# Optimization experiments

Hardware: AMD Instinct MI355X
Metric: run time of the kernel (lower is better)

## Reference

```python
import jax, jax.numpy as jnp
import numpy as np

N = 4096   # num ROIs across the batch (sgdet: ~8 images x 512 proposals)
H = 256    # rl_input_size == rl_hidden_size (hard-coded in __init__)
C = 151    # Visual Genome object classes incl. background


def setup_inputs() -> dict:
    key = jax.random.key(0)
    ks = jax.random.split(key, 7)
    prepro_feat = jax.random.normal(ks[0], (N, H), jnp.float32)
    d = jax.random.uniform(ks[1], (N, C), jnp.float32)
    obj_distributions = d / d.sum(-1, keepdims=True)  # softmax-like class probs
    co_occour = jax.random.uniform(ks[2], (C, C), jnp.float32)
    W_sub = jax.random.normal(ks[3], (H, H), jnp.float32) / np.sqrt(H)
    b_sub = jnp.zeros((H,), jnp.float32)
    W_obj = jax.random.normal(ks[4], (H, H), jnp.float32) / np.sqrt(H)
    b_obj = jnp.zeros((H,), jnp.float32)
    w_scores = jax.random.normal(ks[5], (3 * H + 3,), jnp.float32) / np.sqrt(3 * H + 3)
    b_scores = jnp.zeros((), jnp.float32)
    return dict(prepro_feat=prepro_feat, obj_distributions=obj_distributions,
                co_occour=co_occour, W_sub=W_sub, b_sub=b_sub,
                W_obj=W_obj, b_obj=b_obj, w_scores=w_scores, b_scores=b_scores)


def reference(prepro_feat, obj_distributions, co_occour, W_sub, b_sub,
              W_obj, b_obj, w_scores, b_scores):
    n = prepro_feat.shape[0]
    h = W_sub.shape[1]
    # label_scores = co_occour.sum(1)
    label_scores = co_occour.sum(1)                                   # [C]
    # rl_sub/rl_obj Linear + ReLU. In the torch expand, pair (i,j) uses sub[j], obj[i].
    sub = jax.nn.relu(prepro_feat @ W_sub + b_sub)                    # [N,H]
    obj = jax.nn.relu(prepro_feat @ W_obj + b_obj)                    # [N,H]
    # pair_score[i,j] = sum_{a,b} dist[j,a] * dist[i,b] * co[a,b]  (detached)
    pair_score = jax.lax.stop_gradient(
        jnp.einsum('ja,ab,ib->ij', obj_distributions, co_occour, obj_distributions))  # [N,N]
    s = jax.lax.stop_gradient(obj_distributions @ label_scores)       # [N]
    sub_score = s[None, :]   # varies along j
    obj_score = s[:, None]   # varies along i
    # rl_scores Linear over concat(sub*obj, sub, obj, pair, sub_score, obj_score),
    # decomposed exactly into its blocks (avoids the [N,N,3H+3] intermediate).
    w_mul, w_s, w_o = w_scores[:h], w_scores[h:2 * h], w_scores[2 * h:3 * h]
    w_ps, w_ss, w_os = w_scores[3 * h], w_scores[3 * h + 1], w_scores[3 * h + 2]
    pair_out = ((obj * w_mul) @ sub.T                                 # [i,j] = sum_h obj[i,h]*sub[j,h]*w_mul[h]
                + (sub @ w_s)[None, :]
                + (obj @ w_o)[:, None]
                + w_ps * pair_score + w_ss * sub_score + w_os * obj_score
                + b_scores)                                           # [N,N]
    pair_gates = jax.nn.sigmoid(pair_out).reshape(-1, 1)              # [N*N, 1]
    return pair_gates
```

## Files before the change

kernel.cpp:

```cpp
#include <hip/hip_runtime.h>
#include <hip/hip_bf16.h>
#include <math.h>

#define N_DIM 4096
#define H_DIM 256
#define C_DIM 151
#define KP    448
#define KT    160

typedef unsigned short ushort_t;
typedef __attribute__((ext_vector_type(8))) short bf16x8;
typedef __attribute__((ext_vector_type(4))) float f32x4;

#define WSB_PPACK  0
#define WSB_WT     2097152
#define WSB_DPACK  2359296
#define WSB_COT    3670016
#define WSB_PART   3731456
#define WSB_SPART  3993600
#define WSB_APACK  4091904
#define WSB_BPACK  7761920

#define GLL(src, dst) __builtin_amdgcn_global_load_lds( \
    (const __attribute__((address_space(1))) void*)(src), \
    (__attribute__((address_space(3))) void*)(dst), 16, 0, 0)

__global__ __launch_bounds__(256) void k_cvt(
    const float* __restrict__ P, const float* __restrict__ Ws,
    const float* __restrict__ Wo, const float* __restrict__ D,
    const float* __restrict__ co, const float* __restrict__ wsc,
    __hip_bfloat16* __restrict__ Pp, __hip_bfloat16* __restrict__ Wt,
    __hip_bfloat16* __restrict__ Dpack, __hip_bfloat16* __restrict__ coT,
    __hip_bfloat16* __restrict__ Apack) {
    __shared__ float shbuf[64 * C_DIM];
    const int t = threadIdx.x;
    const int bid = blockIdx.x;
    if (bid < 512) {
        int idx = (bid * 256 + t) * 8;
        float4 a = *(const float4*)(P + idx);
        float4 b = *(const float4*)(P + idx + 4);
        __hip_bfloat16 h[8];
        h[0] = __float2bfloat16(a.x); h[1] = __float2bfloat16(a.y);
        h[2] = __float2bfloat16(a.z); h[3] = __float2bfloat16(a.w);
        h[4] = __float2bfloat16(b.x); h[5] = __float2bfloat16(b.y);
        h[6] = __float2bfloat16(b.z); h[7] = __float2bfloat16(b.w);
        *(bf16x8*)&Pp[idx] = *(bf16x8*)h;
    } else if (bid < 544) {
        const int b  = bid - 512;
        const int k0 = (b & 3) * 64;
        const int h0 = ((b >> 2) & 3) * 64;
        const int z  = b >> 4;
        const float* W = z ? Wo : Ws;
        #pragma unroll
        for (int q = 0; q < 4; ++q) {
            int r = (t >> 4) + q * 16;
            int c = (t & 15) * 4;
            float4 f = *(const float4*)&W[(size_t)(k0 + r) * H_DIM + h0 + c];
            shbuf[r * 65 + c] = f.x; shbuf[r * 65 + c + 1] = f.y;
            shbuf[r * 65 + c + 2] = f.z; shbuf[r * 65 + c + 3] = f.w;
        }
        __syncthreads();
        #pragma unroll
        for (int q = 0; q < 2; ++q) {
            int idx = t + q * 256;
            int h   = idx >> 3;
            int kc  = idx & 7;
            __hip_bfloat16 u[8];
            #pragma unroll
            for (int j = 0; j < 8; ++j)
                u[j] = __float2bfloat16(shbuf[(kc * 8 + j) * 65 + h]);
            *(bf16x8*)&Wt[((size_t)z * H_DIM + h0 + h) * H_DIM + k0 + kc * 8] = *(bf16x8*)u;
        }
    } else if (bid < 608) {
        const int b  = bid - 544;
        const int i0 = b * 64;
        for (int idx = t; idx < 64 * C_DIM; idx += 256)
            shbuf[idx] = D[(size_t)i0 * C_DIM + idx];
        __syncthreads();
        const float wps = wsc[768];
        for (int o = t; o < 64 * (KT / 8); o += 256) {
            int r = o / (KT / 8), ch = o % (KT / 8);
            __hip_bfloat16 u[8];
            #pragma unroll
            for (int j = 0; j < 8; ++j) {
                int k = ch * 8 + j;
                u[j] = __float2bfloat16(k < C_DIM ? shbuf[r * C_DIM + k] : 0.f);
            }
            *(bf16x8*)&Dpack[(size_t)(i0 + r) * KT + ch * 8] = *(bf16x8*)u;
        }
        for (int o = t; o < 64 * 24; o += 256) {
            int r = o / 24, ch = o % 24;
            __hip_bfloat16 u[8];
            #pragma unroll
            for (int j = 0; j < 8; ++j) {
                int c = ch * 8 + j;
                u[j] = __float2bfloat16(c < C_DIM ? wps * shbuf[r * C_DIM + c] : 0.f);
            }
            *(bf16x8*)&Apack[(size_t)(i0 + r) * KP + H_DIM + ch * 8] = *(bf16x8*)u;
        }
    } else {
        const int q  = bid - 608;
        const int a0 = (q % 3) * 64;
        const int c0 = (q / 3) * 64;
        for (int o = t; o < 64 * 64; o += 256) {
            int r = o >> 6, c = o & 63;
            float v = 0.f;
            if (a0 + r < C_DIM && c0 + c < C_DIM)
                v = co[(size_t)(a0 + r) * C_DIM + c0 + c];
            shbuf[r * 65 + c] = v;
        }
        __syncthreads();
        const int nch = (a0 == 128) ? 4 : 8;
        for (int o = t; o < 64 * 8; o += 256) {
            int cl = o >> 3, ch = o & 7;
            if (ch < nch) {
                __hip_bfloat16 u[8];
                #pragma unroll
                for (int j = 0; j < 8; ++j)
                    u[j] = __float2bfloat16(shbuf[(ch * 8 + j) * 65 + cl]);
                *(bf16x8*)&coT[(size_t)(c0 + cl) * KT + a0 + ch * 8] = *(bf16x8*)u;
            }
        }
    }
}

__global__ __launch_bounds__(256) void k_tailmm(
    const ushort_t* __restrict__ Dpack, const ushort_t* __restrict__ coT,
    __hip_bfloat16* __restrict__ Bpack, float* __restrict__ spart) {
    const int t = threadIdx.x;
    const int w = t >> 6, l = t & 63;
    const int wr = w >> 1, wc = w & 1;
    const int lr = l & 15, g = l >> 4;
    const int j0 = blockIdx.x * 64;
    const int i0 = blockIdx.y * 64;

    bf16x8 a[2][5], b[2][5];
    #pragma unroll
    for (int m = 0; m < 2; ++m) {
        const ushort_t* ap = Dpack + (size_t)(i0 + wr * 32 + m * 16 + lr) * KT + g * 8;
        #pragma unroll
        for (int ks = 0; ks < 5; ++ks) a[m][ks] = *(const bf16x8*)(ap + ks * 32);
    }
    #pragma unroll
    for (int n = 0; n < 2; ++n) {
        const ushort_t* bp = coT + (size_t)(j0 + wc * 32 + n * 16 + lr) * KT + g * 8;
        #pragma unroll
        for (int ks = 0; ks < 5; ++ks) b[n][ks] = *(const bf16x8*)(bp + ks * 32);
    }

    f32x4 acc[2][2];
    #pragma unroll
    for (int m = 0; m < 2; ++m)
        #pragma unroll
        for (int n = 0; n < 2; ++n) acc[m][n] = f32x4{0.f, 0.f, 0.f, 0.f};
    #pragma unroll
    for (int ks = 0; ks < 5; ++ks)
        #pragma unroll
        for (int m = 0; m < 2; ++m)
            #pragma unroll
            for (int n = 0; n < 2; ++n)
                acc[m][n] = __builtin_amdgcn_mfma_f32_16x16x32_bf16(
                    a[m][ks], b[n][ks], acc[m][n], 0, 0, 0);

    float* sp = spart + (size_t)(blockIdx.x * 2 + wc) * N_DIM;
    #pragma unroll
    for (int m = 0; m < 2; ++m) {
        float p[4] = {0.f, 0.f, 0.f, 0.f};
        #pragma unroll
        for (int n = 0; n < 2; ++n) {
            int col = j0 + wc * 32 + n * 16 + lr;
            #pragma unroll
            for (int r = 0; r < 4; ++r) {
                int i = i0 + wr * 32 + m * 16 + g * 4 + r;
                float v = acc[m][n][r];
                Bpack[(size_t)i * KP + H_DIM + col] = __float2bfloat16(v);
                p[r] += v;
            }
        }
        #pragma unroll
        for (int r = 0; r < 4; ++r) {
            p[r] += __shfl_xor(p[r], 1);
            p[r] += __shfl_xor(p[r], 2);
            p[r] += __shfl_xor(p[r], 4);
            p[r] += __shfl_xor(p[r], 8);
        }
        if (lr == 0)
            #pragma unroll
            for (int r = 0; r < 4; ++r)
                sp[i0 + wr * 32 + m * 16 + g * 4 + r] = p[r];
    }
}

__global__ __launch_bounds__(256) void k_subobj(
    const ushort_t* __restrict__ Pp, const ushort_t* __restrict__ Wt,
    const float* __restrict__ bsub, const float* __restrict__ bobj,
    const float* __restrict__ wsc,
    __hip_bfloat16* __restrict__ Apack, __hip_bfloat16* __restrict__ Bpack,
    float* __restrict__ part) {
    const int hblk = blockIdx.x;
    const int i0   = blockIdx.y * 128;
    const int z    = blockIdx.z;
    const int j0   = hblk * 64;
    const float* bias = z ? bobj : bsub;
    const ushort_t* Wz = Wt + (size_t)z * H_DIM * H_DIM;

    __shared__ ushort_t As[128 * 256];
    __shared__ ushort_t Bs[64 * 256];

    const int t = threadIdx.x;
    const int w = t >> 6, l = t & 63;
    const int wr = w >> 1, wc = w & 1;
    const int lr = l & 15, g = l >> 4;

    #pragma unroll
    for (int r_ = 0; r_ < 16; ++r_) {
        int idx = t + r_ * 256, row = idx >> 5, cl = idx & 31;
        int cs = cl ^ (row & 7);
        GLL(Pp + (size_t)(i0 + row) * H_DIM + cs * 8, &As[idx * 8]);
    }
    #pragma unroll
    for (int r_ = 0; r_ < 8; ++r_) {
        int idx = t + r_ * 256, row = idx >> 5, cl = idx & 31;
        int cs = cl ^ (row & 7);
        GLL(Wz + (size_t)(j0 + row) * H_DIM + cs * 8, &Bs[idx * 8]);
    }
    __syncthreads();

    f32x4 acc[4][2];
    #pragma unroll
    for (int m = 0; m < 4; ++m)
        #pragma unroll
        for (int n = 0; n < 2; ++n) acc[m][n] = f32x4{0.f, 0.f, 0.f, 0.f};

    #pragma unroll
    for (int ks2 = 0; ks2 < 8; ++ks2) {
        bf16x8 a[4], b[2];
        int c = ks2 * 4 + g;
        #pragma unroll
        for (int m = 0; m < 4; ++m) {
            int Rl = wr * 64 + m * 16 + lr;
            int cl = c ^ (Rl & 7);
            a[m] = *(const bf16x8*)&As[(Rl * 32 + cl) * 8];
        }
        #pragma unroll
        for (int n = 0; n < 2; ++n) {
            int Rl = wc * 32 + n * 16 + lr;
            int cl = c ^ (Rl & 7);
            b[n] = *(const bf16x8*)&Bs[(Rl * 32 + cl) * 8];
        }
        #pragma unroll
        for (int m = 0; m < 4; ++m)
            #pragma unroll
            for (int n = 0; n < 2; ++n)
                acc[m][n] = __builtin_amdgcn_mfma_f32_16x16x32_bf16(
                    a[m], b[n], acc[m][n], 0, 0, 0);
    }

    int hn[2]; float bb[2], wse[2], wmu[2];
    #pragma unroll
    for (int n = 0; n < 2; ++n) {
        hn[n]  = j0 + wc * 32 + n * 16 + lr;
        bb[n]  = bias[hn[n]];
        wse[n] = wsc[(z ? 512 : 256) + hn[n]];
        wmu[n] = wsc[hn[n]];
    }
    float* partq = part + (size_t)(z * 8 + hblk * 2 + wc) * N_DIM;
    #pragma unroll
    for (int m = 0; m < 4; ++m) {
        float p[4] = {0.f, 0.f, 0.f, 0.f};
        #pragma unroll
        for (int n = 0; n < 2; ++n)
            #pragma unroll
            for (int r = 0; r < 4; ++r) {
                float v = acc[m][n][r] + bb[n];
                v = v > 0.f ? v : 0.f;
                int i = i0 + wr * 64 + m * 16 + g * 4 + r;
                if (z) Apack[(size_t)i * KP + hn[n]] = __float2bfloat16(v * wmu[n]);
                else   Bpack[(size_t)i * KP + hn[n]] = __float2bfloat16(v);
                p[r] += v * wse[n];
            }
        #pragma unroll
        for (int r = 0; r < 4; ++r) {
            p[r] += __shfl_xor(p[r], 1);
            p[r] += __shfl_xor(p[r], 2);
            p[r] += __shfl_xor(p[r], 4);
            p[r] += __shfl_xor(p[r], 8);
        }
        if (lr == 0)
            #pragma unroll
            for (int r = 0; r < 4; ++r)
                partq[i0 + wr * 64 + m * 16 + g * 4 + r] = p[r];
    }
}

__global__ __launch_bounds__(512, 2) void k_main(
    const ushort_t* __restrict__ Apack, const ushort_t* __restrict__ Bpack,
    const float* __restrict__ part, const float* __restrict__ spart,
    const float* __restrict__ wsc, const float* __restrict__ bsc,
    float* __restrict__ out) {
    __shared__ ushort_t pool[2][2][256 * 64];
    __shared__ float rbS[256], cbS[256];

    const int t = threadIdx.x;
    const int w = t >> 6, l = t & 63;
    const int wm = w >> 2, wn = w & 3;
    const int lr = l & 15, g = l >> 4;
    const int bid = blockIdx.x;
    const int swz = (bid & 7) * 32 + (bid >> 3);
    const int i0 = (swz >> 4) * 256;
    const int j0 = (swz & 15) * 256;

#define K_STAGE(buf, ks) do {                                                   \
    _Pragma("unroll")                                                           \
    for (int r_ = 0; r_ < 4; ++r_) {                                            \
        int idx_ = t + r_ * 512, row_ = idx_ >> 3, cl_ = idx_ & 7;              \
        int cs_ = cl_ ^ (row_ & 7);                                             \
        GLL(Apack + (size_t)(i0+row_)*KP + (ks)*64 + cs_*8, &pool[buf][0][idx_*8]); \
        GLL(Bpack + (size_t)(j0+row_)*KP + (ks)*64 + cs_*8, &pool[buf][1][idx_*8]); \
    }                                                                           \
} while (0)

    K_STAGE(0, 0);
    if (t < 256) {
        int i = i0 + t; float r = 0.f, si = 0.f;
        #pragma unroll
        for (int q = 8; q < 16; ++q) r += part[(size_t)q * N_DIM + i];
        #pragma unroll
        for (int q = 0; q < 6; ++q) si += spart[(size_t)q * N_DIM + i];
        rbS[t] = r + wsc[770] * si;
    } else {
        int j = j0 + (t - 256); float c = 0.f, sj = 0.f;
        #pragma unroll
        for (int q = 0; q < 8; ++q) c += part[(size_t)q * N_DIM + j];
        #pragma unroll
        for (int q = 0; q < 6; ++q) sj += spart[(size_t)q * N_DIM + j];
        cbS[t - 256] = c + wsc[769] * sj + bsc[0];
    }
    __syncthreads();

    f32x4 acc[8][4];
    #pragma unroll
    for (int m = 0; m < 8; ++m)
        #pragma unroll
        for (int n = 0; n < 4; ++n) acc[m][n] = f32x4{0.f, 0.f, 0.f, 0.f};

    for (int ks = 0; ks < 7; ++ks) {
        const int cur = ks & 1;
        if (ks < 6) K_STAGE(cur ^ 1, ks + 1);
        #pragma unroll
        for (int ks2 = 0; ks2 < 2; ++ks2) {
            bf16x8 a[8], b[4];
            int c = ks2 * 4 + g;
            #pragma unroll
            for (int m = 0; m < 8; ++m) {
                int Rl = wm * 128 + m * 16 + lr;
                int cl = c ^ (Rl & 7);
                a[m] = *(const bf16x8*)&pool[cur][0][(Rl * 8 + cl) * 8];
            }
            #pragma unroll
            for (int n = 0; n < 4; ++n) {
                int Rl = wn * 64 + n * 16 + lr;
                int cl = c ^ (Rl & 7);
                b[n] = *(const bf16x8*)&pool[cur][1][(Rl * 8 + cl) * 8];
            }
            #pragma unroll
            for (int m = 0; m < 8; ++m)
                #pragma unroll
                for (int n = 0; n < 4; ++n)
                    acc[m][n] = __builtin_amdgcn_mfma_f32_16x16x32_bf16(
                        a[m], b[n], acc[m][n], 0, 0, 0);
        }
        __syncthreads();
    }
#undef K_STAGE

    float cbv[4];
    #pragma unroll
    for (int n = 0; n < 4; ++n) cbv[n] = cbS[wn * 64 + n * 16 + lr];
    float* OutS = (float*)pool;
    #pragma unroll
    for (int m = 0; m < 8; ++m) {
        #pragma unroll
        for (int n = 0; n < 4; ++n) {
            #pragma unroll
            for (int r = 0; r < 4; ++r) {
                float rb = rbS[wm * 128 + m * 16 + g * 4 + r];
                float v  = acc[m][n][r] + rb + cbv[n];
                float e  = __expf(-v);
                OutS[(wm * 16 + g * 4 + r) * 260 + wn * 64 + n * 16 + lr] =
                    __builtin_amdgcn_rcpf(1.0f + e);
            }
        }
        __syncthreads();
        {
            int rl = t >> 4, c16 = t & 15;
            int gr = i0 + (rl >> 4) * 128 + m * 16 + (rl & 15);
            float* op = out + (size_t)gr * N_DIM + j0;
            const float* rp = OutS + rl * 260;
            #pragma unroll
            for (int k = 0; k < 4; ++k) {
                float4 v4 = *(const float4*)(rp + (c16 + 16 * k) * 4);
                *(float4*)(op + (c16 + 16 * k) * 4) = v4;
            }
        }
        __syncthreads();
    }
}

extern "C" void kernel_launch(void* const* d_in, const int* in_sizes, int n_in,
                              void* d_out, int out_size, void* d_ws, size_t ws_size,
                              hipStream_t stream) {
    const float* prepro = (const float*)d_in[0];
    const float* D      = (const float*)d_in[1];
    const float* co     = (const float*)d_in[2];
    const float* Wsub   = (const float*)d_in[3];
    const float* bsub   = (const float*)d_in[4];
    const float* Wobj   = (const float*)d_in[5];
    const float* bobj   = (const float*)d_in[6];
    const float* wsc    = (const float*)d_in[7];
    const float* bsc    = (const float*)d_in[8];
    float* out = (float*)d_out;

    char* ws = (char*)d_ws;
    __hip_bfloat16* Ppack = (__hip_bfloat16*)(ws + WSB_PPACK);
    __hip_bfloat16* Wt    = (__hip_bfloat16*)(ws + WSB_WT);
    __hip_bfloat16* Dpack = (__hip_bfloat16*)(ws + WSB_DPACK);
    __hip_bfloat16* coT   = (__hip_bfloat16*)(ws + WSB_COT);
    float* part  = (float*)(ws + WSB_PART);
    float* spart = (float*)(ws + WSB_SPART);
    __hip_bfloat16* Apack = (__hip_bfloat16*)(ws + WSB_APACK);
    __hip_bfloat16* Bpack = (__hip_bfloat16*)(ws + WSB_BPACK);

    k_cvt<<<617, 256, 0, stream>>>(prepro, Wsub, Wobj, D, co, wsc,
                                   Ppack, Wt, Dpack, coT, Apack);
    k_tailmm<<<dim3(3, 64), 256, 0, stream>>>(
        (const ushort_t*)Dpack, (const ushort_t*)coT, Bpack, spart);
    k_subobj<<<dim3(4, N_DIM / 128, 2), 256, 0, stream>>>(
        (const ushort_t*)Ppack, (const ushort_t*)Wt, bsub, bobj, wsc,
        Apack, Bpack, part);
    k_main<<<256, 512, 0, stream>>>(
        (const ushort_t*)Apack, (const ushort_t*)Bpack, part, spart, wsc, bsc, out);
}
```

Measured before the change: 49.53 us.

## Merge tail and sub/obj GEMM kernels, shrink main tile to 256x128

Fuses the pair-score tail GEMM and the sub/obj linear kernels into one launch, using block-index ranges to pick the role. This removes a kernel launch and lets the two independent GEMMs run side by side. The main kernel tile changes from 256x256 to 256x128 with 512 blocks, which halves accumulator registers and LDS per block so more blocks fit per CU, at the cost of more redundant A-tile loads. The rewrite also drops the minimum-blocks hint in launch_bounds.

```diff
diff --git a/kernel.cpp b/kernel.cpp
--- a/kernel.cpp
+++ b/kernel.cpp
@@ -124,199 +124,202 @@
     }
 }
 
-__global__ __launch_bounds__(256) void k_tailmm(
+__global__ __launch_bounds__(256) void k_mid(
+    const ushort_t* __restrict__ Pp, const ushort_t* __restrict__ Wt,
     const ushort_t* __restrict__ Dpack, const ushort_t* __restrict__ coT,
-    __hip_bfloat16* __restrict__ Bpack, float* __restrict__ spart) {
+    const float* __restrict__ bsub, const float* __restrict__ bobj,
+    const float* __restrict__ wsc,
+    __hip_bfloat16* __restrict__ Apack, __hip_bfloat16* __restrict__ Bpack,
+    float* __restrict__ part, float* __restrict__ spart) {
+    __shared__ ushort_t As[128 * 256];
+    __shared__ ushort_t Bs[64 * 256];
+
     const int t = threadIdx.x;
     const int w = t >> 6, l = t & 63;
     const int wr = w >> 1, wc = w & 1;
     const int lr = l & 15, g = l >> 4;
-    const int j0 = blockIdx.x * 64;
-    const int i0 = blockIdx.y * 64;
-
-    bf16x8 a[2][5], b[2][5];
-    #pragma unroll
-    for (int m = 0; m < 2; ++m) {
-        const ushort_t* ap = Dpack + (size_t)(i0 + wr * 32 + m * 16 + lr) * KT + g * 8;
-        #pragma unroll
-        for (int ks = 0; ks < 5; ++ks) a[m][ks] = *(const bf16x8*)(ap + ks * 32);
-    }
-    #pragma unroll
-    for (int n = 0; n < 2; ++n) {
-        const ushort_t* bp = coT + (size_t)(j0 + wc * 32 + n * 16 + lr) * KT + g * 8;
-        #pragma unroll
-        for (int ks = 0; ks < 5; ++ks) b[n][ks] = *(const bf16x8*)(bp + ks * 32);
-    }
-
-    f32x4 acc[2][2];
-    #pragma unroll
-    for (int m = 0; m < 2; ++m)
-        #pragma unroll
-        for (int n = 0; n < 2; ++n) acc[m][n] = f32x4{0.f, 0.f, 0.f, 0.f};
-    #pragma unroll
-    for (int ks = 0; ks < 5; ++ks)
+    const int bid = blockIdx.x;
+
+    if (bid < 256) {
+        const int hblk = bid & 3;
+        const int i0   = ((bid >> 2) & 31) * 128;
+        const int z    = bid >> 7;
+        const int j0   = hblk * 64;
+        const float* bias = z ? bobj : bsub;
+        const ushort_t* Wz = Wt + (size_t)z * H_DIM * H_DIM;
+
+        #pragma unroll
+        for (int r_ = 0; r_ < 16; ++r_) {
+            int idx = t + r_ * 256, row = idx >> 5, cl = idx & 31;
+            int cs = cl ^ (row & 7);
+            GLL(Pp + (size_t)(i0 + row) * H_DIM + cs * 8, &As[idx * 8]);
+        }
+        #pragma unroll
+        for (int r_ = 0; r_ < 8; ++r_) {
+            int idx = t + r_ * 256, row = idx >> 5, cl = idx & 31;
+            int cs = cl ^ (row & 7);
+            GLL(Wz + (size_t)(j0 + row) * H_DIM + cs * 8, &Bs[idx * 8]);
+        }
+        __syncthreads();
+
+        f32x4 acc[4][2];
+        #pragma unroll
+        for (int m = 0; m < 4; ++m)
+            #pragma unroll
+            for (int n = 0; n < 2; ++n) acc[m][n] = f32x4{0.f, 0.f, 0.f, 0.f};
+
+        #pragma unroll
+        for (int ks2 = 0; ks2 < 8; ++ks2) {
+            bf16x8 a[4], b[2];
+            int c = ks2 * 4 + g;
+            #pragma unroll
+            for (int m = 0; m < 4; ++m) {
+                int Rl = wr * 64 + m * 16 + lr;
+                int cl = c ^ (Rl & 7);
+                a[m] = *(const bf16x8*)&As[(Rl * 32 + cl) * 8];
+            }
+            #pragma unroll
+            for (int n = 0; n < 2; ++n) {
+                int Rl = wc * 32 + n * 16 + lr;
+                int cl = c ^ (Rl & 7);
+                b[n] = *(const bf16x8*)&Bs[(Rl * 32 + cl) * 8];
+            }
+            #pragma unroll
+            for (int m = 0; m < 4; ++m)
+                #pragma unroll
+                for (int n = 0; n < 2; ++n)
+                    acc[m][n] = __builtin_amdgcn_mfma_f32_16x16x32_bf16(
+                        a[m], b[n], acc[m][n], 0, 0, 0);
+        }
+
+        int hn[2]; float bb[2], wse[2], wmu[2];
+        #pragma unroll
+        for (int n = 0; n < 2; ++n) {
+            hn[n]  = j0 + wc * 32 + n * 16 + lr;
+            bb[n]  = bias[hn[n]];
+            wse[n] = wsc[(z ? 512 : 256) + hn[n]];
+            wmu[n] = wsc[hn[n]];
+        }
+        float* partq = part + (size_t)(z * 8 + hblk * 2 + wc) * N_DIM;
+        #pragma unroll
+        for (int m = 0; m < 4; ++m) {
+            float p[4] = {0.f, 0.f, 0.f, 0.f};
+            #pragma unroll
+            for (int n = 0; n < 2; ++n)
+                #pragma unroll
+                for (int r = 0; r < 4; ++r) {
+                    float v = acc[m][n][r] + bb[n];
+                    v = v > 0.f ? v : 0.f;
+                    int i = i0 + wr * 64 + m * 16 + g * 4 + r;
+                    if (z) Apack[(size_t)i * KP + hn[n]] = __float2bfloat16(v * wmu[n]);
+                    else   Bpack[(size_t)i * KP + hn[n]] = __float2bfloat16(v);
+                    p[r] += v * wse[n];
+                }
+            #pragma unroll
+            for (int r = 0; r < 4; ++r) {
+                p[r] += __shfl_xor(p[r], 1);
+                p[r] += __shfl_xor(p[r], 2);
+                p[r] += __shfl_xor(p[r], 4);
+                p[r] += __shfl_xor(p[r], 8);
+            }
+            if (lr == 0)
+                #pragma unroll
+                for (int r = 0; r < 4; ++r)
+                    partq[i0 + wr * 64 + m * 16 + g * 4 + r] = p[r];
+        }
+    } else {
+        const int q  = bid - 256;
+        const int j0 = (q % 3) * 64;
+        const int i0 = (q / 3) * 64;
+
+        bf16x8 a[2][5], b[2][5];
+        #pragma unroll
+        for (int m = 0; m < 2; ++m) {
+            const ushort_t* ap = Dpack + (size_t)(i0 + wr * 32 + m * 16 + lr) * KT + g * 8;
+            #pragma unroll
+            for (int ks = 0; ks < 5; ++ks) a[m][ks] = *(const bf16x8*)(ap + ks * 32);
+        }
+        #pragma unroll
+        for (int n = 0; n < 2; ++n) {
+            const ushort_t* bp = coT + (size_t)(j0 + wc * 32 + n * 16 + lr) * KT + g * 8;
+            #pragma unroll
+            for (int ks = 0; ks < 5; ++ks) b[n][ks] = *(const bf16x8*)(bp + ks * 32);
+        }
+
+        f32x4 acc[2][2];
         #pragma unroll
         for (int m = 0; m < 2; ++m)
             #pragma unroll
-            for (int n = 0; n < 2; ++n)
-                acc[m][n] = __builtin_amdgcn_mfma_f32_16x16x32_bf16(
-                    a[m][ks], b[n][ks], acc[m][n], 0, 0, 0);
-
-    float* sp = spart + (size_t)(blockIdx.x * 2 + wc) * N_DIM;
-    #pragma unroll
-    for (int m = 0; m < 2; ++m) {
-        float p[4] = {0.f, 0.f, 0.f, 0.f};
-        #pragma unroll
-        for (int n = 0; n < 2; ++n) {
-            int col = j0 + wc * 32 + n * 16 + lr;
+            for (int n = 0; n < 2; ++n) acc[m][n] = f32x4{0.f, 0.f, 0.f, 0.f};
+        #pragma unroll
+        for (int ks = 0; ks < 5; ++ks)
+            #pragma unroll
+            for (int m = 0; m < 2; ++m)
+                #pragma unroll
+                for (int n = 0; n < 2; ++n)
+                    acc[m][n] = __builtin_amdgcn_mfma_f32_16x16x32_bf16(
+                        a[m][ks], b[n][ks], acc[m][n], 0, 0, 0);
+
+        float* sp = spart + (size_t)((q % 3) * 2 + wc) * N_DIM;
+        #pragma unroll
+        for (int m = 0; m < 2; ++m) {
+            float p[4] = {0.f, 0.f, 0.f, 0.f};
+            #pragma unroll
+            for (int n = 0; n < 2; ++n) {
+                int col = j0 + wc * 32 + n * 16 + lr;
+                #pragma unroll
+                for (int r = 0; r < 4; ++r) {
+                    int i = i0 + wr * 32 + m * 16 + g * 4 + r;
+                    float v = acc[m][n][r];
+                    Bpack[(size_t)i * KP + H_DIM + col] = __float2bfloat16(v);
+                    p[r] += v;
+                }
+            }
             #pragma unroll
             for (int r = 0; r < 4; ++r) {
-                int i = i0 + wr * 32 + m * 16 + g * 4 + r;
-                float v = acc[m][n][r];
-                Bpack[(size_t)i * KP + H_DIM + col] = __float2bfloat16(v);
-                p[r] += v;
-            }
-        }
-        #pragma unroll
-        for (int r = 0; r < 4; ++r) {
-            p[r] += __shfl_xor(p[r], 1);
-            p[r] += __shfl_xor(p[r], 2);
-            p[r] += __shfl_xor(p[r], 4);
-            p[r] += __shfl_xor(p[r], 8);
-        }
-        if (lr == 0)
-            #pragma unroll
-            for (int r = 0; r < 4; ++r)
-                sp[i0 + wr * 32 + m * 16 + g * 4 + r] = p[r];
+                p[r] += __shfl_xor(p[r], 1);
+                p[r] += __shfl_xor(p[r], 2);
+                p[r] += __shfl_xor(p[r], 4);
+                p[r] += __shfl_xor(p[r], 8);
+            }
+            if (lr == 0)
+                #pragma unroll
+                for (int r = 0; r < 4; ++r)
+                    sp[i0 + wr * 32 + m * 16 + g * 4 + r] = p[r];
+        }
     }
 }
 
-__global__ __launch_bounds__(256) void k_subobj(
-    const ushort_t* __restrict__ Pp, const ushort_t* __restrict__ Wt,
-    const float* __restrict__ bsub, const float* __restrict__ bobj,
-    const float* __restrict__ wsc,
-    __hip_bfloat16* __restrict__ Apack, __hip_bfloat16* __restrict__ Bpack,
-    float* __restrict__ part) {
-    const int hblk = blockIdx.x;
-    const int i0   = blockIdx.y * 128;
-    const int z    = blockIdx.z;
-    const int j0   = hblk * 64;
-    const float* bias = z ? bobj : bsub;
-    const ushort_t* Wz = Wt + (size_t)z * H_DIM * H_DIM;
-
-    __shared__ ushort_t As[128 * 256];
-    __shared__ ushort_t Bs[64 * 256];
-
-    const int t = threadIdx.x;
-    const int w = t >> 6, l = t & 63;
-    const int wr = w >> 1, wc = w & 1;
-    const int lr = l & 15, g = l >> 4;
-
-    #pragma unroll
-    for (int r_ = 0; r_ < 16; ++r_) {
-        int idx = t + r_ * 256, row = idx >> 5, cl = idx & 31;
-        int cs = cl ^ (row & 7);
-        GLL(Pp + (size_t)(i0 + row) * H_DIM + cs * 8, &As[idx * 8]);
-    }
-    #pragma unroll
-    for (int r_ = 0; r_ < 8; ++r_) {
-        int idx = t + r_ * 256, row = idx >> 5, cl = idx & 31;
-        int cs = cl ^ (row & 7);
-        GLL(Wz + (size_t)(j0 + row) * H_DIM + cs * 8, &Bs[idx * 8]);
-    }
-    __syncthreads();
-
-    f32x4 acc[4][2];
-    #pragma unroll
-    for (int m = 0; m < 4; ++m)
-        #pragma unroll
-        for (int n = 0; n < 2; ++n) acc[m][n] = f32x4{0.f, 0.f, 0.f, 0.f};
-
-    #pragma unroll
-    for (int ks2 = 0; ks2 < 8; ++ks2) {
-        bf16x8 a[4], b[2];
-        int c = ks2 * 4 + g;
-        #pragma unroll
-        for (int m = 0; m < 4; ++m) {
-            int Rl = wr * 64 + m * 16 + lr;
-            int cl = c ^ (Rl & 7);
-            a[m] = *(const bf16x8*)&As[(Rl * 32 + cl) * 8];
-        }
-        #pragma unroll
-        for (int n = 0; n < 2; ++n) {
-            int Rl = wc * 32 + n * 16 + lr;
-            int cl = c ^ (Rl & 7);
-            b[n] = *(const bf16x8*)&Bs[(Rl * 32 + cl) * 8];
-        }
-        #pragma unroll
-        for (int m = 0; m < 4; ++m)
-            #pragma unroll
-            for (int n = 0; n < 2; ++n)
-                acc[m][n] = __builtin_amdgcn_mfma_f32_16x16x32_bf16(
-                    a[m], b[n], acc[m][n], 0, 0, 0);
-    }
-
-    int hn[2]; float bb[2], wse[2], wmu[2];
-    #pragma unroll
-    for (int n = 0; n < 2; ++n) {
-        hn[n]  = j0 + wc * 32 + n * 16 + lr;
-        bb[n]  = bias[hn[n]];
-        wse[n] = wsc[(z ? 512 : 256) + hn[n]];
-        wmu[n] = wsc[hn[n]];
-    }
-    float* partq = part + (size_t)(z * 8 + hblk * 2 + wc) * N_DIM;
-    #pragma unroll
-    for (int m = 0; m < 4; ++m) {
-        float p[4] = {0.f, 0.f, 0.f, 0.f};
-        #pragma unroll
-        for (int n = 0; n < 2; ++n)
-            #pragma unroll
-            for (int r = 0; r < 4; ++r) {
-                float v = acc[m][n][r] + bb[n];
-                v = v > 0.f ? v : 0.f;
-                int i = i0 + wr * 64 + m * 16 + g * 4 + r;
-                if (z) Apack[(size_t)i * KP + hn[n]] = __float2bfloat16(v * wmu[n]);
-                else   Bpack[(size_t)i * KP + hn[n]] = __float2bfloat16(v);
-                p[r] += v * wse[n];
-            }
-        #pragma unroll
-        for (int r = 0; r < 4; ++r) {
-            p[r] += __shfl_xor(p[r], 1);
-            p[r] += __shfl_xor(p[r], 2);
-            p[r] += __shfl_xor(p[r], 4);
-            p[r] += __shfl_xor(p[r], 8);
-        }
-        if (lr == 0)
-            #pragma unroll
-            for (int r = 0; r < 4; ++r)
-                partq[i0 + wr * 64 + m * 16 + g * 4 + r] = p[r];
-    }
-}
-
-__global__ __launch_bounds__(512, 2) void k_main(
+__global__ __launch_bounds__(512) void k_main(
     const ushort_t* __restrict__ Apack, const ushort_t* __restrict__ Bpack,
     const float* __restrict__ part, const float* __restrict__ spart,
     const float* __restrict__ wsc, const float* __restrict__ bsc,
     float* __restrict__ out) {
-    __shared__ ushort_t pool[2][2][256 * 64];
-    __shared__ float rbS[256], cbS[256];
+    __shared__ ushort_t pa[2][256 * 64];
+    __shared__ ushort_t pb[2][128 * 64];
+    __shared__ float rbS[256], cbS[128];
 
     const int t = threadIdx.x;
     const int w = t >> 6, l = t & 63;
-    const int wm = w >> 2, wn = w & 3;
+    const int wm = w >> 1, wn = w & 1;
     const int lr = l & 15, g = l >> 4;
     const int bid = blockIdx.x;
-    const int swz = (bid & 7) * 32 + (bid >> 3);
-    const int i0 = (swz >> 4) * 256;
-    const int j0 = (swz & 15) * 256;
+    const int wgid = (bid & 7) * 64 + (bid >> 3);
+    const int i0 = (wgid >> 5) * 256;
+    const int j0 = (wgid & 31) * 128;
 
 #define K_STAGE(buf, ks) do {                                                   \
     _Pragma("unroll")                                                           \
     for (int r_ = 0; r_ < 4; ++r_) {                                            \
         int idx_ = t + r_ * 512, row_ = idx_ >> 3, cl_ = idx_ & 7;              \
         int cs_ = cl_ ^ (row_ & 7);                                             \
-        GLL(Apack + (size_t)(i0+row_)*KP + (ks)*64 + cs_*8, &pool[buf][0][idx_*8]); \
-        GLL(Bpack + (size_t)(j0+row_)*KP + (ks)*64 + cs_*8, &pool[buf][1][idx_*8]); \
+        GLL(Apack + (size_t)(i0+row_)*KP + (ks)*64 + cs_*8, &pa[buf][idx_*8]);  \
+    }                                                                           \
+    _Pragma("unroll")                                                           \
+    for (int r_ = 0; r_ < 2; ++r_) {                                            \
+        int idx_ = t + r_ * 512, row_ = idx_ >> 3, cl_ = idx_ & 7;              \
+        int cs_ = cl_ ^ (row_ & 7);                                             \
+        GLL(Bpack + (size_t)(j0+row_)*KP + (ks)*64 + cs_*8, &pb[buf][idx_*8]);  \
     }                                                                           \
 } while (0)
 
@@ -328,7 +331,7 @@
         #pragma unroll
         for (int q = 0; q < 6; ++q) si += spart[(size_t)q * N_DIM + i];
         rbS[t] = r + wsc[770] * si;
-    } else {
+    } else if (t < 384) {
         int j = j0 + (t - 256); float c = 0.f, sj = 0.f;
         #pragma unroll
         for (int q = 0; q < 8; ++q) c += part[(size_t)q * N_DIM + j];
@@ -338,9 +341,9 @@
     }
     __syncthreads();
 
-    f32x4 acc[8][4];
+    f32x4 acc[4][4];
     #pragma unroll
-    for (int m = 0; m < 8; ++m)
+    for (int m = 0; m < 4; ++m)
         #pragma unroll
         for (int n = 0; n < 4; ++n) acc[m][n] = f32x4{0.f, 0.f, 0.f, 0.f};
 
@@ -349,22 +352,22 @@
         if (ks < 6) K_STAGE(cur ^ 1, ks + 1);
         #pragma unroll
         for (int ks2 = 0; ks2 < 2; ++ks2) {
-            bf16x8 a[8], b[4];
+            bf16x8 a[4], b[4];
             int c = ks2 * 4 + g;
             #pragma unroll
-            for (int m = 0; m < 8; ++m) {
-                int Rl = wm * 128 + m * 16 + lr;
+            for (int m = 0; m < 4; ++m) {
+                int Rl = wm * 64 + m * 16 + lr;
                 int cl = c ^ (Rl & 7);
-                a[m] = *(const bf16x8*)&pool[cur][0][(Rl * 8 + cl) * 8];
+                a[m] = *(const bf16x8*)&pa[cur][(Rl * 8 + cl) * 8];
             }
             #pragma unroll
             for (int n = 0; n < 4; ++n) {
                 int Rl = wn * 64 + n * 16 + lr;
                 int cl = c ^ (Rl & 7);
-                b[n] = *(const bf16x8*)&pool[cur][1][(Rl * 8 + cl) * 8];
-            }
-            #pragma unroll
-            for (int m = 0; m < 8; ++m)
+                b[n] = *(const bf16x8*)&pb[cur][(Rl * 8 + cl) * 8];
+            }
+            #pragma unroll
+            for (int m = 0; m < 4; ++m)
                 #pragma unroll
                 for (int n = 0; n < 4; ++n)
                     acc[m][n] = __builtin_amdgcn_mfma_f32_16x16x32_bf16(
@@ -377,30 +380,30 @@
     float cbv[4];
     #pragma unroll
     for (int n = 0; n < 4; ++n) cbv[n] = cbS[wn * 64 + n * 16 + lr];
-    float* OutS = (float*)pool;
+    float* OutS = (float*)pa;
     #pragma unroll
-    for (int m = 0; m < 8; ++m) {
+    for (int m = 0; m < 4; ++m) {
         #pragma unroll
         for (int n = 0; n < 4; ++n) {
             #pragma unroll
             for (int r = 0; r < 4; ++r) {
-                float rb = rbS[wm * 128 + m * 16 + g * 4 + r];
+                float rb = rbS[wm * 64 + m * 16 + g * 4 + r];
                 float v  = acc[m][n][r] + rb + cbv[n];
                 float e  = __expf(-v);
-                OutS[(wm * 16 + g * 4 + r) * 260 + wn * 64 + n * 16 + lr] =
+                OutS[(wm * 16 + g * 4 + r) * 132 + wn * 64 + n * 16 + lr] =
                     __builtin_amdgcn_rcpf(1.0f + e);
             }
         }
         __syncthreads();
         {
-            int rl = t >> 4, c16 = t & 15;
-            int gr = i0 + (rl >> 4) * 128 + m * 16 + (rl & 15);
+            int rl = t >> 3, c8 = t & 7;
+            int gr = i0 + (rl >> 4) * 64 + m * 16 + (rl & 15);
             float* op = out + (size_t)gr * N_DIM + j0;
-            const float* rp = OutS + rl * 260;
+            const float* rp = OutS + rl * 132;
             #pragma unroll
             for (int k = 0; k < 4; ++k) {
-                float4 v4 = *(const float4*)(rp + (c16 + 16 * k) * 4);
-                *(float4*)(op + (c16 + 16 * k) * 4) = v4;
+                float4 v4 = *(const float4*)(rp + (c8 + 8 * k) * 4);
+                *(float4*)(op + (c8 + 8 * k) * 4) = v4;
             }
         }
         __syncthreads();
@@ -433,11 +436,10 @@
 
     k_cvt<<<617, 256, 0, stream>>>(prepro, Wsub, Wobj, D, co, wsc,
                                    Ppack, Wt, Dpack, coT, Apack);
-    k_tailmm<<<dim3(3, 64), 256, 0, stream>>>(
-        (const ushort_t*)Dpack, (const ushort_t*)coT, Bpack, spart);
-    k_subobj<<<dim3(4, N_DIM / 128, 2), 256, 0, stream>>>(
-        (const ushort_t*)Ppack, (const ushort_t*)Wt, bsub, bobj, wsc,
-        Apack, Bpack, part);
-    k_main<<<256, 512, 0, stream>>>(
+    k_mid<<<448, 256, 0, stream>>>(
+        (const ushort_t*)Ppack, (const ushort_t*)Wt,
+        (const ushort_t*)Dpack, (const ushort_t*)coT,
+        bsub, bobj, wsc, Apack, Bpack, part, spart);
+    k_main<<<512, 512, 0, stream>>>(
         (const ushort_t*)Apack, (const ushort_t*)Bpack, part, spart, wsc, bsc, out);
 }
```

Result: slower. 54.15 us (+9.3%).

## Merge tail and sub/obj GEMM kernels; use explicit waitcnt barriers in main loop

Applied to the files above, without the earlier changes.

Merges the pair-score tail GEMM and the sub/obj linear GEMM into one kernel, split by block index, so a single launch covers both and their blocks can run concurrently. In the main kernel it replaces __syncthreads with explicit vmcnt waits plus raw s_barrier and sched_barrier, and peels the last K step out of the loop. The goal is to drop a launch gap and let the next tile's loads stay in flight during compute. The hand-counted vmcnt(8) ties correctness to the exact number of loads each K_STAGE issues, so any change in that count would break the synchronisation.

```diff
diff --git a/kernel.cpp b/kernel.cpp
--- a/kernel.cpp
+++ b/kernel.cpp
@@ -124,172 +124,169 @@
     }
 }
 
-__global__ __launch_bounds__(256) void k_tailmm(
+__global__ __launch_bounds__(256) void k_mid(
+    const ushort_t* __restrict__ Pp, const ushort_t* __restrict__ Wt,
     const ushort_t* __restrict__ Dpack, const ushort_t* __restrict__ coT,
-    __hip_bfloat16* __restrict__ Bpack, float* __restrict__ spart) {
+    const float* __restrict__ bsub, const float* __restrict__ bobj,
+    const float* __restrict__ wsc,
+    __hip_bfloat16* __restrict__ Apack, __hip_bfloat16* __restrict__ Bpack,
+    float* __restrict__ part, float* __restrict__ spart) {
+    __shared__ ushort_t As[128 * 256];
+    __shared__ ushort_t Bs[64 * 256];
+
     const int t = threadIdx.x;
     const int w = t >> 6, l = t & 63;
     const int wr = w >> 1, wc = w & 1;
     const int lr = l & 15, g = l >> 4;
-    const int j0 = blockIdx.x * 64;
-    const int i0 = blockIdx.y * 64;
-
-    bf16x8 a[2][5], b[2][5];
-    #pragma unroll
-    for (int m = 0; m < 2; ++m) {
-        const ushort_t* ap = Dpack + (size_t)(i0 + wr * 32 + m * 16 + lr) * KT + g * 8;
-        #pragma unroll
-        for (int ks = 0; ks < 5; ++ks) a[m][ks] = *(const bf16x8*)(ap + ks * 32);
-    }
-    #pragma unroll
-    for (int n = 0; n < 2; ++n) {
-        const ushort_t* bp = coT + (size_t)(j0 + wc * 32 + n * 16 + lr) * KT + g * 8;
-        #pragma unroll
-        for (int ks = 0; ks < 5; ++ks) b[n][ks] = *(const bf16x8*)(bp + ks * 32);
-    }
-
-    f32x4 acc[2][2];
-    #pragma unroll
-    for (int m = 0; m < 2; ++m)
-        #pragma unroll
-        for (int n = 0; n < 2; ++n) acc[m][n] = f32x4{0.f, 0.f, 0.f, 0.f};
-    #pragma unroll
-    for (int ks = 0; ks < 5; ++ks)
+    const int bid = blockIdx.x;
+
+    if (bid < 256) {
+        const int hblk = bid & 3;
+        const int i0   = ((bid >> 2) & 31) * 128;
+        const int z    = bid >> 7;
+        const int j0   = hblk * 64;
+        const float* bias = z ? bobj : bsub;
+        const ushort_t* Wz = Wt + (size_t)z * H_DIM * H_DIM;
+
+        #pragma unroll
+        for (int r_ = 0; r_ < 16; ++r_) {
+            int idx = t + r_ * 256, row = idx >> 5, cl = idx & 31;
+            int cs = cl ^ (row & 7);
+            GLL(Pp + (size_t)(i0 + row) * H_DIM + cs * 8, &As[idx * 8]);
+        }
+        #pragma unroll
+        for (int r_ = 0; r_ < 8; ++r_) {
+            int idx = t + r_ * 256, row = idx >> 5, cl = idx & 31;
+            int cs = cl ^ (row & 7);
+            GLL(Wz + (size_t)(j0 + row) * H_DIM + cs * 8, &Bs[idx * 8]);
+        }
+        __syncthreads();
+
+        f32x4 acc[4][2];
+        #pragma unroll
+        for (int m = 0; m < 4; ++m)
+            #pragma unroll
+            for (int n = 0; n < 2; ++n) acc[m][n] = f32x4{0.f, 0.f, 0.f, 0.f};
+
+        #pragma unroll
+        for (int ks2 = 0; ks2 < 8; ++ks2) {
+            bf16x8 a[4], b[2];
+            int c = ks2 * 4 + g;
+            #pragma unroll
+            for (int m = 0; m < 4; ++m) {
+                int Rl = wr * 64 + m * 16 + lr;
+                int cl = c ^ (Rl & 7);
+                a[m] = *(const bf16x8*)&As[(Rl * 32 + cl) * 8];
+            }
+            #pragma unroll
+            for (int n = 0; n < 2; ++n) {
+                int Rl = wc * 32 + n * 16 + lr;
+                int cl = c ^ (Rl & 7);
+                b[n] = *(const bf16x8*)&Bs[(Rl * 32 + cl) * 8];
+            }
+            #pragma unroll
+            for (int m = 0; m < 4; ++m)
+                #pragma unroll
+                for (int n = 0; n < 2; ++n)
+                    acc[m][n] = __builtin_amdgcn_mfma_f32_16x16x32_bf16(
+                        a[m], b[n], acc[m][n], 0, 0, 0);
+        }
+
+        int hn[2]; float bb[2], wse[2], wmu[2];
+        #pragma unroll
+        for (int n = 0; n < 2; ++n) {
+            hn[n]  = j0 + wc * 32 + n * 16 + lr;
+            bb[n]  = bias[hn[n]];
+            wse[n] = wsc[(z ? 512 : 256) + hn[n]];
+            wmu[n] = wsc[hn[n]];
+        }
+        float* partq = part + (size_t)(z * 8 + hblk * 2 + wc) * N_DIM;
+        #pragma unroll
+        for (int m = 0; m < 4; ++m) {
+            float p[4] = {0.f, 0.f, 0.f, 0.f};
+            #pragma unroll
+            for (int n = 0; n < 2; ++n)
+                #pragma unroll
+                for (int r = 0; r < 4; ++r) {
+                    float v = acc[m][n][r] + bb[n];
+                    v = v > 0.f ? v : 0.f;
+                    int i = i0 + wr * 64 + m * 16 + g * 4 + r;
+                    if (z) Apack[(size_t)i * KP + hn[n]] = __float2bfloat16(v * wmu[n]);
+                    else   Bpack[(size_t)i * KP + hn[n]] = __float2bfloat16(v);
+                    p[r] += v * wse[n];
+                }
+            #pragma unroll
+            for (int r = 0; r < 4; ++r) {
+                p[r] += __shfl_xor(p[r], 1);
+                p[r] += __shfl_xor(p[r], 2);
+                p[r] += __shfl_xor(p[r], 4);
+                p[r] += __shfl_xor(p[r], 8);
+            }
+            if (lr == 0)
+                #pragma unroll
+                for (int r = 0; r < 4; ++r)
+                    partq[i0 + wr * 64 + m * 16 + g * 4 + r] = p[r];
+        }
+    } else {
+        const int q  = bid - 256;
+        const int j0 = (q % 3) * 64;
+        const int i0 = (q / 3) * 64;
+
+        bf16x8 a[2][5], b[2][5];
+        #pragma unroll
+        for (int m = 0; m < 2; ++m) {
+            const ushort_t* ap = Dpack + (size_t)(i0 + wr * 32 + m * 16 + lr) * KT + g * 8;
+            #pragma unroll
+            for (int ks = 0; ks < 5; ++ks) a[m][ks] = *(const bf16x8*)(ap + ks * 32);
+        }
+        #pragma unroll
+        for (int n = 0; n < 2; ++n) {
+            const ushort_t* bp = coT + (size_t)(j0 + wc * 32 + n * 16 + lr) * KT + g * 8;
+            #pragma unroll
+            for (int ks = 0; ks < 5; ++ks) b[n][ks] = *(const bf16x8*)(bp + ks * 32);
+        }
+
+        f32x4 acc[2][2];
         #pragma unroll
         for (int m = 0; m < 2; ++m)
             #pragma unroll
-            for (int n = 0; n < 2; ++n)
-                acc[m][n] = __builtin_amdgcn_mfma_f32_16x16x32_bf16(
-                    a[m][ks], b[n][ks], acc[m][n], 0, 0, 0);
-
-    float* sp = spart + (size_t)(blockIdx.x * 2 + wc) * N_DIM;
-    #pragma unroll
-    for (int m = 0; m < 2; ++m) {
-        float p[4] = {0.f, 0.f, 0.f, 0.f};
-        #pragma unroll
-        for (int n = 0; n < 2; ++n) {
-            int col = j0 + wc * 32 + n * 16 + lr;
+            for (int n = 0; n < 2; ++n) acc[m][n] = f32x4{0.f, 0.f, 0.f, 0.f};
+        #pragma unroll
+        for (int ks = 0; ks < 5; ++ks)
+            #pragma unroll
+            for (int m = 0; m < 2; ++m)
+                #pragma unroll
+                for (int n = 0; n < 2; ++n)
+                    acc[m][n] = __builtin_amdgcn_mfma_f32_16x16x32_bf16(
+                        a[m][ks], b[n][ks], acc[m][n], 0, 0, 0);
+
+        float* sp = spart + (size_t)((q % 3) * 2 + wc) * N_DIM;
+        #pragma unroll
+        for (int m = 0; m < 2; ++m) {
+            float p[4] = {0.f, 0.f, 0.f, 0.f};
+            #pragma unroll
+            for (int n = 0; n < 2; ++n) {
+                int col = j0 + wc * 32 + n * 16 + lr;
+                #pragma unroll
+                for (int r = 0; r < 4; ++r) {
+                    int i = i0 + wr * 32 + m * 16 + g * 4 + r;
+                    float v = acc[m][n][r];
+                    Bpack[(size_t)i * KP + H_DIM + col] = __float2bfloat16(v);
+                    p[r] += v;
+                }
+            }
             #pragma unroll
             for (int r = 0; r < 4; ++r) {
-                int i = i0 + wr * 32 + m * 16 + g * 4 + r;
-                float v = acc[m][n][r];
-                Bpack[(size_t)i * KP + H_DIM + col] = __float2bfloat16(v);
-                p[r] += v;
-            }
-        }
-        #pragma unroll
-        for (int r = 0; r < 4; ++r) {
-            p[r] += __shfl_xor(p[r], 1);
-            p[r] += __shfl_xor(p[r], 2);
-            p[r] += __shfl_xor(p[r], 4);
-            p[r] += __shfl_xor(p[r], 8);
-        }
-        if (lr == 0)
-            #pragma unroll
-            for (int r = 0; r < 4; ++r)
-                sp[i0 + wr * 32 + m * 16 + g * 4 + r] = p[r];
-    }
-}
-
-__global__ __launch_bounds__(256) void k_subobj(
-    const ushort_t* __restrict__ Pp, const ushort_t* __restrict__ Wt,
-    const float* __restrict__ bsub, const float* __restrict__ bobj,
-    const float* __restrict__ wsc,
-    __hip_bfloat16* __restrict__ Apack, __hip_bfloat16* __restrict__ Bpack,
-    float* __restrict__ part) {
-    const int hblk = blockIdx.x;
-    const int i0   = blockIdx.y * 128;
-    const int z    = blockIdx.z;
-    const int j0   = hblk * 64;
-    const float* bias = z ? bobj : bsub;
-    const ushort_t* Wz = Wt + (size_t)z * H_DIM * H_DIM;
-
-    __shared__ ushort_t As[128 * 256];
-    __shared__ ushort_t Bs[64 * 256];
-
-    const int t = threadIdx.x;
-    const int w = t >> 6, l = t & 63;
-    const int wr = w >> 1, wc = w & 1;
-    const int lr = l & 15, g = l >> 4;
-
-    #pragma unroll
-    for (int r_ = 0; r_ < 16; ++r_) {
-        int idx = t + r_ * 256, row = idx >> 5, cl = idx & 31;
-        int cs = cl ^ (row & 7);
-        GLL(Pp + (size_t)(i0 + row) * H_DIM + cs * 8, &As[idx * 8]);
-    }
-    #pragma unroll
-    for (int r_ = 0; r_ < 8; ++r_) {
-        int idx = t + r_ * 256, row = idx >> 5, cl = idx & 31;
-        int cs = cl ^ (row & 7);
-        GLL(Wz + (size_t)(j0 + row) * H_DIM + cs * 8, &Bs[idx * 8]);
-    }
-    __syncthreads();
-
-    f32x4 acc[4][2];
-    #pragma unroll
-    for (int m = 0; m < 4; ++m)
-        #pragma unroll
-        for (int n = 0; n < 2; ++n) acc[m][n] = f32x4{0.f, 0.f, 0.f, 0.f};
-
-    #pragma unroll
-    for (int ks2 = 0; ks2 < 8; ++ks2) {
-        bf16x8 a[4], b[2];
-        int c = ks2 * 4 + g;
-        #pragma unroll
-        for (int m = 0; m < 4; ++m) {
-            int Rl = wr * 64 + m * 16 + lr;
-            int cl = c ^ (Rl & 7);
-            a[m] = *(const bf16x8*)&As[(Rl * 32 + cl) * 8];
-        }
-        #pragma unroll
-        for (int n = 0; n < 2; ++n) {
-            int Rl = wc * 32 + n * 16 + lr;
-            int cl = c ^ (Rl & 7);
-            b[n] = *(const bf16x8*)&Bs[(Rl * 32 + cl) * 8];
-        }
-        #pragma unroll
-        for (int m = 0; m < 4; ++m)
-            #pragma unroll
-            for (int n = 0; n < 2; ++n)
-                acc[m][n] = __builtin_amdgcn_mfma_f32_16x16x32_bf16(
-                    a[m], b[n], acc[m][n], 0, 0, 0);
-    }
-
-    int hn[2]; float bb[2], wse[2], wmu[2];
-    #pragma unroll
-    for (int n = 0; n < 2; ++n) {
-        hn[n]  = j0 + wc * 32 + n * 16 + lr;
-        bb[n]  = bias[hn[n]];
-        wse[n] = wsc[(z ? 512 : 256) + hn[n]];
-        wmu[n] = wsc[hn[n]];
-    }
-    float* partq = part + (size_t)(z * 8 + hblk * 2 + wc) * N_DIM;
-    #pragma unroll
-    for (int m = 0; m < 4; ++m) {
-        float p[4] = {0.f, 0.f, 0.f, 0.f};
-        #pragma unroll
-        for (int n = 0; n < 2; ++n)
-            #pragma unroll
-            for (int r = 0; r < 4; ++r) {
-                float v = acc[m][n][r] + bb[n];
-                v = v > 0.f ? v : 0.f;
-                int i = i0 + wr * 64 + m * 16 + g * 4 + r;
-                if (z) Apack[(size_t)i * KP + hn[n]] = __float2bfloat16(v * wmu[n]);
-                else   Bpack[(size_t)i * KP + hn[n]] = __float2bfloat16(v);
-                p[r] += v * wse[n];
-            }
-        #pragma unroll
-        for (int r = 0; r < 4; ++r) {
-            p[r] += __shfl_xor(p[r], 1);
-            p[r] += __shfl_xor(p[r], 2);
-            p[r] += __shfl_xor(p[r], 4);
-            p[r] += __shfl_xor(p[r], 8);
-        }
-        if (lr == 0)
-            #pragma unroll
-            for (int r = 0; r < 4; ++r)
-                partq[i0 + wr * 64 + m * 16 + g * 4 + r] = p[r];
+                p[r] += __shfl_xor(p[r], 1);
+                p[r] += __shfl_xor(p[r], 2);
+                p[r] += __shfl_xor(p[r], 4);
+                p[r] += __shfl_xor(p[r], 8);
+            }
+            if (lr == 0)
+                #pragma unroll
+                for (int r = 0; r < 4; ++r)
+                    sp[i0 + wr * 32 + m * 16 + g * 4 + r] = p[r];
+        }
     }
 }
 
@@ -320,6 +317,32 @@
     }                                                                           \
 } while (0)
 
+#define K_COMPUTE(cur) do {                                                     \
+    _Pragma("unroll")                                                           \
+    for (int ks2 = 0; ks2 < 2; ++ks2) {                                         \
+        bf16x8 a[8], b[4];                                                      \
+        int c = ks2 * 4 + g;                                                    \
+        _Pragma("unroll")                                                       \
+        for (int m = 0; m < 8; ++m) {                                           \
+            int Rl = wm * 128 + m * 16 + lr;                                    \
+            int cl = c ^ (Rl & 7);                                              \
+            a[m] = *(const bf16x8*)&pool[cur][0][(Rl * 8 + cl) * 8];            \
+        }                                                                       \
+        _Pragma("unroll")                                                       \
+        for (int n = 0; n < 4; ++n) {                                           \
+            int Rl = wn * 64 + n * 16 + lr;                                     \
+            int cl = c ^ (Rl & 7);                                              \
+            b[n] = *(const bf16x8*)&pool[cur][1][(Rl * 8 + cl) * 8];            \
+        }                                                                       \
+        _Pragma("unroll")                                                       \
+        for (int m = 0; m < 8; ++m)                                             \
+            _Pragma("unroll")                                                   \
+            for (int n = 0; n < 4; ++n)                                         \
+                acc[m][n] = __builtin_amdgcn_mfma_f32_16x16x32_bf16(            \
+                    a[m], b[n], acc[m][n], 0, 0, 0);                            \
+    }                                                                           \
+} while (0)
+
     K_STAGE(0, 0);
     if (t < 256) {
         int i = i0 + t; float r = 0.f, si = 0.f;
@@ -344,35 +367,24 @@
         #pragma unroll
         for (int n = 0; n < 4; ++n) acc[m][n] = f32x4{0.f, 0.f, 0.f, 0.f};
 
-    for (int ks = 0; ks < 7; ++ks) {
+    for (int ks = 0; ks < 6; ++ks) {
         const int cur = ks & 1;
-        if (ks < 6) K_STAGE(cur ^ 1, ks + 1);
-        #pragma unroll
-        for (int ks2 = 0; ks2 < 2; ++ks2) {
-            bf16x8 a[8], b[4];
-            int c = ks2 * 4 + g;
-            #pragma unroll
-            for (int m = 0; m < 8; ++m) {
-                int Rl = wm * 128 + m * 16 + lr;
-                int cl = c ^ (Rl & 7);
-                a[m] = *(const bf16x8*)&pool[cur][0][(Rl * 8 + cl) * 8];
-            }
-            #pragma unroll
-            for (int n = 0; n < 4; ++n) {
-                int Rl = wn * 64 + n * 16 + lr;
-                int cl = c ^ (Rl & 7);
-                b[n] = *(const bf16x8*)&pool[cur][1][(Rl * 8 + cl) * 8];
-            }
-            #pragma unroll
-            for (int m = 0; m < 8; ++m)
-                #pragma unroll
-                for (int n = 0; n < 4; ++n)
-                    acc[m][n] = __builtin_amdgcn_mfma_f32_16x16x32_bf16(
-                        a[m], b[n], acc[m][n], 0, 0, 0);
-        }
-        __syncthreads();
+        K_STAGE(cur ^ 1, ks + 1);
+        asm volatile("s_waitcnt vmcnt(8)" ::: "memory");
+        __builtin_amdgcn_s_barrier();
+        __builtin_amdgcn_sched_barrier(0);
+        K_COMPUTE(cur);
+        __builtin_amdgcn_s_barrier();
+        __builtin_amdgcn_sched_barrier(0);
     }
+    asm volatile("s_waitcnt vmcnt(0)" ::: "memory");
+    __builtin_amdgcn_s_barrier();
+    __builtin_amdgcn_sched_barrier(0);
+    K_COMPUTE(0);
+    __builtin_amdgcn_s_barrier();
+    __builtin_amdgcn_sched_barrier(0);
 #undef K_STAGE
+#undef K_COMPUTE
 
     float cbv[4];
     #pragma unroll
@@ -391,7 +403,9 @@
                     __builtin_amdgcn_rcpf(1.0f + e);
             }
         }
-        __syncthreads();
+        asm volatile("s_waitcnt lgkmcnt(0)" ::: "memory");
+        __builtin_amdgcn_s_barrier();
+        __builtin_amdgcn_sched_barrier(0);
         {
             int rl = t >> 4, c16 = t & 15;
             int gr = i0 + (rl >> 4) * 128 + m * 16 + (rl & 15);
@@ -403,7 +417,8 @@
                 *(float4*)(op + (c16 + 16 * k) * 4) = v4;
             }
         }
-        __syncthreads();
+        __builtin_amdgcn_s_barrier();
+        __builtin_amdgcn_sched_barrier(0);
     }
 }
 
@@ -433,11 +448,10 @@
 
     k_cvt<<<617, 256, 0, stream>>>(prepro, Wsub, Wobj, D, co, wsc,
                                    Ppack, Wt, Dpack, coT, Apack);
-    k_tailmm<<<dim3(3, 64), 256, 0, stream>>>(
-        (const ushort_t*)Dpack, (const ushort_t*)coT, Bpack, spart);
-    k_subobj<<<dim3(4, N_DIM / 128, 2), 256, 0, stream>>>(
-        (const ushort_t*)Ppack, (const ushort_t*)Wt, bsub, bobj, wsc,
-        Apack, Bpack, part);
+    k_mid<<<448, 256, 0, stream>>>(
+        (const ushort_t*)Ppack, (const ushort_t*)Wt,
+        (const ushort_t*)Dpack, (const ushort_t*)coT,
+        bsub, bobj, wsc, Apack, Bpack, part, spart);
     k_main<<<256, 512, 0, stream>>>(
         (const ushort_t*)Apack, (const ushort_t*)Bpack, part, spart, wsc, bsc, out);
 }
```

Result: no change. 49.22 us (-0.6%).
